# Kernel tuning notes

Hardware: AMD Instinct MI355X
Metric: run time of the kernel (lower is better)

## Reference

```python
import jax, jax.numpy as jnp
import numpy as np

B, N, VD, ED, HD, V, T = 64, 196, 512, 512, 512, 10000, 20


def setup_inputs() -> dict:
    key = jax.random.key(0)
    ks = jax.random.split(key, 12)
    s = lambda k, shape: jax.random.normal(k, shape, jnp.float32) * 0.02
    return {
        "features": jax.random.normal(ks[0], (B, N, VD), jnp.float32),
        "captions": jax.random.randint(ks[1], (B, T), 0, V),
        "W_init_h": s(ks[2], (HD, VD)),
        "W_init_c": s(ks[3], (HD, VD)),
        "W_av": s(ks[4], (1, VD)),
        "b_av": jnp.zeros((1,), jnp.float32),
        "W_ah": s(ks[5], (1, HD)),
        "b_ah": jnp.zeros((1,), jnp.float32),
        "embed": s(ks[6], (V, ED)),
        "W_ih": s(ks[7], (4 * HD, VD + ED)),
        "W_hh": s(ks[8], (4 * HD, HD)),
        "b_ih": jnp.zeros((4 * HD,), jnp.float32),
        "b_hh": jnp.zeros((4 * HD,), jnp.float32),
        "W_out": s(ks[9], (V, HD)),
        "b_out": jnp.zeros((V,), jnp.float32),
    }


def reference(features, captions, W_init_h, W_init_c, W_av, b_av, W_ah, b_ah,
              embed, W_ih, W_hh, b_ih, b_hh, W_out, b_out):
    vis_num = features.shape[1]
    # init hidden/cell: sum over vis_num of Linear(features) / vis_num
    h0 = jnp.einsum('bnv,hv->bh', features, W_init_h) / vis_num  # [B,H]
    c0 = jnp.einsum('bnv,hv->bh', features, W_init_c) / vis_num  # [B,H]
    # word embeddings, time-major: [T,B,E]
    emb = jnp.swapaxes(embed[captions], 0, 1)
    # visual part of additive attention is step-invariant: precompute [B,N,1]
    att_v = jnp.einsum('bnv,ov->bno', features, W_av) + b_av

    def step(carry, e_t):
        h, c = carry
        att_h = h @ W_ah.T + b_ah                          # [B,1]
        attn = jax.nn.softmax(att_v + att_h[:, None, :], axis=1)  # [B,N,1]
        ctx = jnp.sum(features * attn, axis=1)             # [B,VD]
        x = jnp.concatenate([ctx, e_t], axis=1)            # [B,VD+ED]
        gates = x @ W_ih.T + b_ih + h @ W_hh.T + b_hh      # [B,4H]
        i, f, g, o = jnp.split(gates, 4, axis=1)
        c = jax.nn.sigmoid(f) * c + jax.nn.sigmoid(i) * jnp.tanh(g)
        h = jax.nn.sigmoid(o) * jnp.tanh(c)
        words = h @ W_out.T + b_out                        # [B,V]
        return (h, c), words

    _, word_space = jax.lax.scan(step, (h0, c0), emb)      # [T,B,V]
    return jax.nn.log_softmax(word_space, axis=2), jax.nn.softmax(word_space, axis=2)
```

## Files before the change

kernel.cpp:

```cpp
#include <hip/hip_runtime.h>
#include <math.h>

#define B_   64
#define N_   196
#define VD_  512
#define ED_  512
#define HD_  512
#define V_   10000
#define T_   20
#define G4_  2048
#define LSTM_NBLK 32

typedef __attribute__((ext_vector_type(8))) short bf16x8;
typedef __attribute__((ext_vector_type(4))) float f32x4;

static __device__ __forceinline__ float sigmoidf_(float x) {
  return 1.f / (1.f + __expf(-x));
}

static __device__ __forceinline__ float tanh_fast(float x) {
  float e = __expf(2.f * x);
  return 1.f - 2.f / (e + 1.f);
}

static __device__ __forceinline__ unsigned short f2bf_(float x) {
  unsigned u = __float_as_uint(x);
  unsigned r = (u + 0x7FFFu + ((u >> 16) & 1u)) >> 16;
  return (unsigned short)r;
}

__global__ void k_prep(const float* __restrict__ W_out,
                       const float* __restrict__ W_ih,
                       const float* __restrict__ W_hh,
                       const float* __restrict__ embed,
                       const int* __restrict__ caps,
                       const float* __restrict__ feat,
                       const float* __restrict__ W_av,
                       unsigned short* __restrict__ wout_bf,
                       unsigned short* __restrict__ wihe_bf,
                       unsigned short* __restrict__ whh_bf,
                       unsigned short* __restrict__ emb_bf,
                       float* __restrict__ svg) {
  int bx = blockIdx.x, tid = threadIdx.x;
  if (bx >= 7688) {
    int r = bx - 7688;
    int b = r >> 2, q = r & 3;
    int lane = tid & 63, w = tid >> 6;
    const float* fb = feat + (size_t)b * (N_ * VD_);
    float4 wv0 = *(const float4*)(W_av + lane * 8);
    float4 wv1 = *(const float4*)(W_av + lane * 8 + 4);
    int nbase = q * 49;
    for (int n = nbase + w; n < nbase + 49; n += 4) {
      const float* fp = fb + n * VD_ + lane * 8;
      float4 f0 = *(const float4*)fp;
      float4 f1 = *(const float4*)(fp + 4);
      float p = f0.x * wv0.x + f0.y * wv0.y + f0.z * wv0.z + f0.w * wv0.w
              + f1.x * wv1.x + f1.y * wv1.y + f1.z * wv1.z + f1.w * wv1.w;
#pragma unroll
      for (int off = 32; off > 0; off >>= 1) p += __shfl_down(p, off, 64);
      if (lane == 0) svg[b * N_ + n] = p;
    }
    return;
  }
  float4 v; unsigned short* dst; int i;
  if (bx < 5000) {
    i = bx * 256 + tid;
    v = ((const float4*)W_out)[i];
    dst = wout_bf;
  } else if (bx < 6024) {
    i = (bx - 5000) * 256 + tid;
    int j = i >> 7, kk = (i & 127) << 2;
    v = *(const float4*)(W_ih + (size_t)j * (VD_ + ED_) + VD_ + kk);
    dst = wihe_bf;
  } else if (bx < 6664) {
    i = (bx - 6024) * 256 + tid;
    int row = i >> 7;
    int b = row & 63, t = row >> 6;
    v = *(const float4*)(embed + (size_t)caps[b * T_ + t] * ED_ + ((i & 127) << 2));
    dst = emb_bf;
  } else {
    i = (bx - 6664) * 256 + tid;
    v = ((const float4*)W_hh)[i];
    dst = whh_bf;
  }
  ushort4 o;
  o.x = f2bf_(v.x); o.y = f2bf_(v.y); o.z = f2bf_(v.z); o.w = f2bf_(v.w);
  ((ushort4*)dst)[i] = o;
}

__global__ void k_attn2(const float* __restrict__ feat,
                        const float* __restrict__ svg,
                        float* __restrict__ fmean,
                        float* __restrict__ ctx) {
  __shared__ float sa[200];
  __shared__ float red[8];
  __shared__ float pc[2][128];
  __shared__ float pf[2][128];
  int b = blockIdx.x, q = blockIdx.y;
  int tid = threadIdx.x, lane = tid & 63, w = tid >> 6;
  const float* fb = feat + (size_t)b * (N_ * VD_);

  float v = (tid < N_) ? svg[b * N_ + tid] : -1e30f;
  float m = v;
#pragma unroll
  for (int off = 32; off > 0; off >>= 1) m = fmaxf(m, __shfl_down(m, off, 64));
  if (lane == 0) red[w] = m;
  __syncthreads();
  m = fmaxf(fmaxf(red[0], red[1]), fmaxf(red[2], red[3]));

  float e = (tid < N_) ? __expf(v - m) : 0.f;
  float s = e;
#pragma unroll
  for (int off = 32; off > 0; off >>= 1) s += __shfl_down(s, off, 64);
  if (lane == 0) red[4 + w] = s;
  __syncthreads();
  float inv = 1.f / (red[4] + red[5] + red[6] + red[7]);
  if (tid < N_) sa[tid] = e * inv;
  __syncthreads();

  int d = q * 128 + (tid & 127);
  int nh = tid >> 7;
  float c = 0.f, fs = 0.f;
  for (int n = nh; n < N_; n += 2) {
    float f = fb[n * VD_ + d];
    c += sa[n] * f;
    fs += f;
  }
  pc[nh][tid & 127] = c;
  pf[nh][tid & 127] = fs;
  __syncthreads();
  if (tid < 128) {
    ctx[b * VD_ + q * 128 + tid] = pc[0][tid] + pc[1][tid];
    fmean[b * VD_ + q * 128 + tid] = (pf[0][tid] + pf[1][tid]) * (1.f / N_);
  }
}

#define BK 16
__global__ __launch_bounds__(256) void k_small(
    const float* __restrict__ fmean, const float* __restrict__ ctx,
    const float* __restrict__ W_init_h, const float* __restrict__ W_init_c,
    const float* __restrict__ W_ih,
    const float* __restrict__ b_ih, const float* __restrict__ b_hh,
    float* __restrict__ hbuf, float* __restrict__ cbuf, float* __restrict__ gctx,
    unsigned short* __restrict__ h0_bf) {
  const float* A; const float* Bw; float* C;
  int ldb, ldc, n0;
  const float* bias1 = nullptr; const float* bias2 = nullptr;
  unsigned short* hb = nullptr;
  int bx = blockIdx.x;
  if (bx < 8)       { A = fmean; Bw = W_init_h; C = hbuf; ldb = VD_; ldc = HD_; n0 = bx * 64; hb = h0_bf; }
  else if (bx < 16) { A = fmean; Bw = W_init_c; C = cbuf; ldb = VD_; ldc = HD_; n0 = (bx - 8) * 64; }
  else { A = ctx; Bw = W_ih; C = gctx; ldb = VD_ + ED_; ldc = G4_; n0 = (bx - 16) * 64;
         bias1 = b_ih; bias2 = b_hh; }

  __shared__ float As[BK][64];
  __shared__ float Bs[BK][64];
  int tid = threadIdx.x;
  int tm = tid & 15, tn = tid >> 4;
  int sr = tid >> 2, sk = (tid & 3) * 4;
  const float* arow = A + (size_t)sr * VD_;
  const float* brow = Bw + (size_t)(n0 + sr) * ldb;
  float acc[4][4] = {};

  for (int k0 = 0; k0 < VD_; k0 += BK) {
    float4 av = *(const float4*)(arow + k0 + sk);
    float4 bv = *(const float4*)(brow + k0 + sk);
    __syncthreads();
    As[sk + 0][sr] = av.x; As[sk + 1][sr] = av.y;
    As[sk + 2][sr] = av.z; As[sk + 3][sr] = av.w;
    Bs[sk + 0][sr] = bv.x; Bs[sk + 1][sr] = bv.y;
    Bs[sk + 2][sr] = bv.z; Bs[sk + 3][sr] = bv.w;
    __syncthreads();
#pragma unroll
    for (int kk = 0; kk < BK; ++kk) {
      float4 a4 = *(const float4*)&As[kk][tm * 4];
      float4 b4 = *(const float4*)&Bs[kk][tn * 4];
      acc[0][0] += a4.x * b4.x; acc[0][1] += a4.x * b4.y; acc[0][2] += a4.x * b4.z; acc[0][3] += a4.x * b4.w;
      acc[1][0] += a4.y * b4.x; acc[1][1] += a4.y * b4.y; acc[1][2] += a4.y * b4.z; acc[1][3] += a4.y * b4.w;
      acc[2][0] += a4.z * b4.x; acc[2][1] += a4.z * b4.y; acc[2][2] += a4.z * b4.z; acc[2][3] += a4.z * b4.w;
      acc[3][0] += a4.w * b4.x; acc[3][1] += a4.w * b4.y; acc[3][2] += a4.w * b4.z; acc[3][3] += a4.w * b4.w;
    }
  }
#pragma unroll
  for (int j = 0; j < 4; ++j) {
    int n = n0 + tn * 4 + j;
    float bb = (bias1 ? bias1[n] + bias2[n] : 0.f);
#pragma unroll
    for (int i = 0; i < 4; ++i) {
      int mm = tm * 4 + i;
      float val = acc[i][j] + bb;
      C[(size_t)mm * ldc + n] = val;
      if (hb) hb[(size_t)mm * HD_ + n] = f2bf_(val);
    }
  }
}

__global__ __launch_bounds__(256) void k_gemm_mfma(
    const unsigned short* __restrict__ A,
    const unsigned short* __restrict__ Bw,
    const float* __restrict__ bias,
    const float* __restrict__ radd, int ldr,
    float* __restrict__ C, int M, int Nn, int K) {
  __shared__ unsigned short As[128][32];
  __shared__ unsigned short Bs[128][32];
  int tid = threadIdx.x;
  int wave = tid >> 6, lane = tid & 63;
  int wm = wave & 1, wn = wave >> 1;
  int m0 = blockIdx.y * 128, n0 = blockIdx.x * 128;
  int l15 = lane & 15, quad = lane >> 4;
  int sr = tid >> 1, skq = (tid & 1) * 16;
  const unsigned short* ga = A + (size_t)(m0 + sr) * K + skq;
  int bn = n0 + sr; if (bn >= Nn) bn = Nn - 1;
  const unsigned short* gb = Bw + (size_t)bn * K + skq;

  f32x4 acc[4][4];
#pragma unroll
  for (int i = 0; i < 4; ++i)
#pragma unroll
    for (int j = 0; j < 4; ++j) acc[i][j] = (f32x4){0.f, 0.f, 0.f, 0.f};

  for (int k0 = 0; k0 < K; k0 += 32) {
    bf16x8 a0 = *(const bf16x8*)(ga + k0);
    bf16x8 a1 = *(const bf16x8*)(ga + k0 + 8);
    bf16x8 b0 = *(const bf16x8*)(gb + k0);
    bf16x8 b1 = *(const bf16x8*)(gb + k0 + 8);
    __syncthreads();
    *(bf16x8*)&As[sr][skq] = a0; *(bf16x8*)&As[sr][skq + 8] = a1;
    *(bf16x8*)&Bs[sr][skq] = b0; *(bf16x8*)&Bs[sr][skq + 8] = b1;
    __syncthreads();
    bf16x8 af[4], bfr[4];
#pragma unroll
    for (int mt = 0; mt < 4; ++mt)
      af[mt] = *(const bf16x8*)&As[wm * 64 + mt * 16 + l15][quad * 8];
#pragma unroll
    for (int nt = 0; nt < 4; ++nt)
      bfr[nt] = *(const bf16x8*)&Bs[wn * 64 + nt * 16 + l15][quad * 8];
#pragma unroll
    for (int mt = 0; mt < 4; ++mt)
#pragma unroll
      for (int nt = 0; nt < 4; ++nt)
        acc[mt][nt] = __builtin_amdgcn_mfma_f32_16x16x32_bf16(af[mt], bfr[nt], acc[mt][nt], 0, 0, 0);
  }

#pragma unroll
  for (int nt = 0; nt < 4; ++nt) {
    int n = n0 + wn * 64 + nt * 16 + l15;
    if (n < Nn) {
      float bb = bias ? bias[n] : 0.f;
#pragma unroll
      for (int mt = 0; mt < 4; ++mt) {
        int mbase = m0 + wm * 64 + mt * 16 + quad * 4;
#pragma unroll
        for (int r = 0; r < 4; ++r) {
          int mg = mbase + r;
          float ra = radd ? radd[(size_t)(mg & 63) * ldr + n] : 0.f;
          C[(size_t)mg * Nn + n] = acc[mt][nt][r] + bb + ra;
        }
      }
    }
  }
}

__global__ __launch_bounds__(256, 1) void k_lstm_mfma(
    const unsigned short* __restrict__ whh_bf,
    const float* __restrict__ gpre,
    const unsigned short* __restrict__ h0_bf,
    const float* __restrict__ c0,
    unsigned short* __restrict__ hall_bf,
    int* __restrict__ bar) {
  __shared__ unsigned short whh_s[64 * 512];
  int tid = threadIdx.x;
  int w = tid >> 6, lane = tid & 63;
  int l15 = lane & 15, quad = lane >> 4;
  int n0 = blockIdx.x * 16;

  for (int idx = tid; idx < 4096; idx += 256) {
    int r = idx >> 6, gg = idx & 63;
    int gate = r >> 4, l = r & 15;
    bf16x8 v = *(const bf16x8*)(whh_bf +
        (size_t)(gate * HD_ + n0 + l) * HD_ + gg * 8);
    *(bf16x8*)&whh_s[r * 512 + (gg ^ (r & 7)) * 8] = v;
  }

  int brow = w * 16 + quad * 4;

  float c_reg[4];
#pragma unroll
  for (int r = 0; r < 4; ++r)
    c_reg[r] = c0[(size_t)(brow + r) * HD_ + n0 + l15];

  float gr[16];
#pragma unroll
  for (int g = 0; g < 4; ++g)
#pragma unroll
    for (int r = 0; r < 4; ++r)
      gr[g * 4 + r] = gpre[(size_t)(brow + r) * G4_ + g * HD_ + n0 + l15];

  __syncthreads();

  for (int t = 0; t < T_; ++t) {
    const unsigned short* h_in =
        (t == 0) ? h0_bf : (hall_bf + (size_t)(t - 1) * B_ * HD_);
    const unsigned short* ar = h_in + (size_t)(w * 16 + l15) * HD_ + quad * 8;

    bf16x8 a[16];
#pragma unroll
    for (int ki = 0; ki < 16; ++ki) a[ki] = *(const bf16x8*)(ar + ki * 32);

    f32x4 acc[4];
#pragma unroll
    for (int i = 0; i < 4; ++i) acc[i] = (f32x4){0.f, 0.f, 0.f, 0.f};

#pragma unroll
    for (int ki = 0; ki < 16; ++ki) {
      int rb = l15 * 512 + (((ki * 4 + quad) ^ (l15 & 7)) << 3);
#pragma unroll
      for (int nt = 0; nt < 4; ++nt) {
        bf16x8 b = *(const bf16x8*)&whh_s[nt * 16 * 512 + rb];
        acc[nt] = __builtin_amdgcn_mfma_f32_16x16x32_bf16(a[ki], b, acc[nt], 0, 0, 0);
      }
    }

    unsigned short* hout = hall_bf + (size_t)t * B_ * HD_;
#pragma unroll
    for (int r = 0; r < 4; ++r) {
      float gi = acc[0][r] + gr[0 + r];
      float gf = acc[1][r] + gr[4 + r];
      float gg = acc[2][r] + gr[8 + r];
      float go = acc[3][r] + gr[12 + r];
      float cn = sigmoidf_(gf) * c_reg[r] + sigmoidf_(gi) * tanh_fast(gg);
      c_reg[r] = cn;
      hout[(size_t)(brow + r) * HD_ + n0 + l15] =
          f2bf_(sigmoidf_(go) * tanh_fast(cn));
    }

    if (t < T_ - 1) {
      __syncthreads();
      if (tid == 0) {
        __threadfence();
        atomicAdd(bar, 1);
        int target = (t + 1) * LSTM_NBLK;
        while (__hip_atomic_load(bar, __ATOMIC_RELAXED,
                                 __HIP_MEMORY_SCOPE_AGENT) < target)
          __builtin_amdgcn_s_sleep(2);
        __threadfence();
      }
      __syncthreads();
      const float* gpt = gpre + (size_t)(t + 1) * B_ * G4_;
#pragma unroll
      for (int g = 0; g < 4; ++g)
#pragma unroll
        for (int r = 0; r < 4; ++r)
          gr[g * 4 + r] = gpt[(size_t)(brow + r) * G4_ + g * HD_ + n0 + l15];
    }
  }
}

__global__ void k_softmax(float* __restrict__ logits, float* __restrict__ out1) {
  __shared__ float red[8];
  int row = blockIdx.x, tid = threadIdx.x;
  int lane = tid & 63, wid = tid >> 6;
  float* lr = logits + (size_t)row * V_;
  float* o1 = out1 + (size_t)row * V_;
  const int NV4 = V_ / 4;

  float m = -1e30f;
  for (int i = tid; i < NV4; i += 256) {
    float4 v = ((const float4*)lr)[i];
    m = fmaxf(m, fmaxf(fmaxf(v.x, v.y), fmaxf(v.z, v.w)));
  }
#pragma unroll
  for (int off = 32; off > 0; off >>= 1) m = fmaxf(m, __shfl_down(m, off, 64));
  if (lane == 0) red[4 + wid] = m;
  __syncthreads();
  m = fmaxf(fmaxf(red[4], red[5]), fmaxf(red[6], red[7]));

  float s = 0.f;
  for (int i = tid; i < NV4; i += 256) {
    float4 v = ((const float4*)lr)[i];
    s += __expf(v.x - m) + __expf(v.y - m) + __expf(v.z - m) + __expf(v.w - m);
  }
#pragma unroll
  for (int off = 32; off > 0; off >>= 1) s += __shfl_down(s, off, 64);
  if (lane == 0) red[wid] = s;
  __syncthreads();
  s = red[0] + red[1] + red[2] + red[3];
  float ls = __logf(s), inv = 1.f / s;

  for (int i = tid; i < NV4; i += 256) {
    float4 v = ((const float4*)lr)[i];
    float4 a, bb;
    a.x = v.x - m - ls; a.y = v.y - m - ls; a.z = v.z - m - ls; a.w = v.w - m - ls;
    bb.x = __expf(v.x - m) * inv; bb.y = __expf(v.y - m) * inv;
    bb.z = __expf(v.z - m) * inv; bb.w = __expf(v.w - m) * inv;
    ((float4*)o1)[i] = a;
    ((float4*)lr)[i] = bb;
  }
}

extern "C" void kernel_launch(void* const* d_in, const int* in_sizes, int n_in,
                              void* d_out, int out_size, void* d_ws, size_t ws_size,
                              hipStream_t stream) {
  const float* features = (const float*)d_in[0];
  const int*   captions = (const int*)d_in[1];
  const float* W_init_h = (const float*)d_in[2];
  const float* W_init_c = (const float*)d_in[3];
  const float* W_av     = (const float*)d_in[4];
  const float* embed    = (const float*)d_in[8];
  const float* W_ih     = (const float*)d_in[9];
  const float* W_hh     = (const float*)d_in[10];
  const float* b_ih     = (const float*)d_in[11];
  const float* b_hh     = (const float*)d_in[12];
  const float* W_out    = (const float*)d_in[13];
  const float* b_out    = (const float*)d_in[14];

  float* ws    = (float*)d_ws;
  float* fmean = ws;
  float* ctx   = fmean + B_ * VD_;
  float* hbuf  = ctx + B_ * VD_;
  float* cbuf  = hbuf + B_ * HD_;
  float* gctx  = cbuf + B_ * HD_;
  float* svg   = gctx + (size_t)B_ * G4_;
  float* gpre  = svg + 12608;
  int*   bar   = (int*)(gpre + (size_t)T_ * B_ * G4_);
  unsigned short* wout_bf = (unsigned short*)(bar + 64);
  unsigned short* wihe_bf = wout_bf + (size_t)V_ * HD_;
  unsigned short* whh_bf  = wihe_bf + (size_t)G4_ * ED_;
  unsigned short* emb_bf  = whh_bf + (size_t)G4_ * HD_;
  unsigned short* h0_bf   = emb_bf + (size_t)T_ * B_ * ED_;
  unsigned short* hall_bf = h0_bf + (size_t)B_ * HD_;

  float* out1   = (float*)d_out;
  float* logits = out1 + (size_t)T_ * B_ * V_;

  hipMemsetAsync(bar, 0, 256, stream);

  k_prep<<<7944, 256, 0, stream>>>(W_out, W_ih, W_hh, embed, captions,
                                   features, W_av,
                                   wout_bf, wihe_bf, whh_bf, emb_bf, svg);
  k_attn2<<<dim3(B_, 4), 256, 0, stream>>>(features, svg, fmean, ctx);
  k_small<<<48, 256, 0, stream>>>(fmean, ctx, W_init_h, W_init_c, W_ih,
                                  b_ih, b_hh, hbuf, cbuf, gctx, h0_bf);

  k_gemm_mfma<<<dim3(G4_ / 128, (T_ * B_) / 128), 256, 0, stream>>>(
      emb_bf, wihe_bf, nullptr, gctx, G4_, gpre, T_ * B_, G4_, ED_);

  k_lstm_mfma<<<LSTM_NBLK, 256, 0, stream>>>(
      whh_bf, gpre, h0_bf, cbuf, hall_bf, bar);

  k_gemm_mfma<<<dim3((V_ + 127) / 128, (T_ * B_) / 128), 256, 0, stream>>>(
      hall_bf, wout_bf, b_out, nullptr, 0, logits, T_ * B_, V_, HD_);

  k_softmax<<<T_ * B_, 256, 0, stream>>>(logits, out1);
}
```

Before: 502.7 us.

## Replace atomic counter grid barrier with per-block flags and coherent loads/stores

```diff
diff --git a/kernel.cpp b/kernel.cpp
--- a/kernel.cpp
+++ b/kernel.cpp
@@ -305,7 +305,11 @@
 
     bf16x8 a[16];
 #pragma unroll
-    for (int ki = 0; ki < 16; ++ki) a[ki] = *(const bf16x8*)(ar + ki * 32);
+    for (int ki = 0; ki < 16; ++ki)
+      asm volatile("global_load_dwordx4 %0, %1, off sc0 sc1"
+                   : "=v"(a[ki]) : "v"(ar + ki * 32) : "memory");
+    asm volatile("s_waitcnt vmcnt(0)" ::: "memory");
+    __builtin_amdgcn_sched_barrier(0);
 
     f32x4 acc[4];
 #pragma unroll
@@ -330,28 +334,37 @@
       float go = acc[3][r] + gr[12 + r];
       float cn = sigmoidf_(gf) * c_reg[r] + sigmoidf_(gi) * tanh_fast(gg);
       c_reg[r] = cn;
-      hout[(size_t)(brow + r) * HD_ + n0 + l15] =
-          f2bf_(sigmoidf_(go) * tanh_fast(cn));
+      unsigned hv = f2bf_(sigmoidf_(go) * tanh_fast(cn));
+      unsigned short* sp = hout + (size_t)(brow + r) * HD_ + n0 + l15;
+      asm volatile("global_store_short %0, %1, off sc0 sc1"
+                   :: "v"(sp), "v"(hv) : "memory");
     }
 
     if (t < T_ - 1) {
+      asm volatile("s_waitcnt vmcnt(0)" ::: "memory");
       __syncthreads();
       if (tid == 0) {
-        __threadfence();
-        atomicAdd(bar, 1);
-        int target = (t + 1) * LSTM_NBLK;
-        while (__hip_atomic_load(bar, __ATOMIC_RELAXED,
-                                 __HIP_MEMORY_SCOPE_AGENT) < target)
-          __builtin_amdgcn_s_sleep(2);
-        __threadfence();
+        int* fp = bar + blockIdx.x * 16;
+        int fv = t + 1;
+        asm volatile("global_store_dword %0, %1, off sc0 sc1"
+                     :: "v"(fp), "v"(fv) : "memory");
+      }
+      const float* gpt = gpre + (size_t)(t + 1) * B_ * G4_;
+#pragma unroll
+      for (int g = 0; g < 4; ++g)
+#pragma unroll
+        for (int r = 0; r < 4; ++r)
+          gr[g * 4 + r] = gpt[(size_t)(brow + r) * G4_ + g * HD_ + n0 + l15];
+      if (tid < 64) {
+        int* fp = bar + (tid & 31) * 16;
+        while (true) {
+          int v = __hip_atomic_load(fp, __ATOMIC_RELAXED,
+                                    __HIP_MEMORY_SCOPE_AGENT);
+          if (__all(v >= t + 1)) break;
+          __builtin_amdgcn_s_sleep(1);
+        }
       }
       __syncthreads();
-      const float* gpt = gpre + (size_t)(t + 1) * B_ * G4_;
-#pragma unroll
-      for (int g = 0; g < 4; ++g)
-#pragma unroll
-        for (int r = 0; r < 4; ++r)
-          gr[g * 4 + r] = gpt[(size_t)(brow + r) * G4_ + g * HD_ + n0 + l15];
     }
   }
 }
@@ -423,7 +436,7 @@
   float* svg   = gctx + (size_t)B_ * G4_;
   float* gpre  = svg + 12608;
   int*   bar   = (int*)(gpre + (size_t)T_ * B_ * G4_);
-  unsigned short* wout_bf = (unsigned short*)(bar + 64);
+  unsigned short* wout_bf = (unsigned short*)(bar + 512);
   unsigned short* wihe_bf = wout_bf + (size_t)V_ * HD_;
   unsigned short* whh_bf  = wihe_bf + (size_t)G4_ * ED_;
   unsigned short* emb_bf  = whh_bf + (size_t)G4_ * HD_;
@@ -433,7 +446,7 @@
   float* out1   = (float*)d_out;
   float* logits = out1 + (size_t)T_ * B_ * V_;
 
-  hipMemsetAsync(bar, 0, 256, stream);
+  hipMemsetAsync(bar, 0, 2048, stream);
 
   k_prep<<<7944, 256, 0, stream>>>(W_out, W_ih, W_hh, embed, captions,
                                    features, W_av,
```

New measurement: 469.6 us. -6.6%, faster.
